# Kernel optimization log

Hardware: AMD Instinct MI355X
Metric: run time of the kernel (lower is better)

The kernel has to match this reference:

```python
import jax, jax.numpy as jnp
import numpy as np

N_NODES = 50000
N_EDGES = 800000
IN_CH = 128
HID = 128
N_LAYERS = 2


def setup_inputs() -> dict:
    key = jax.random.key(0)
    ks = jax.random.split(key, 8)
    x = jax.random.normal(ks[0], (N_NODES, IN_CH), dtype=jnp.float32)
    edge_index = jax.random.randint(ks[1], (2, N_EDGES), 0, N_NODES, dtype=jnp.int32)
    s = 1.0 / np.sqrt(IN_CH)
    lin_w = jax.random.uniform(ks[2], (IN_CH, HID), jnp.float32, -s, s)
    lin_b = jax.random.uniform(ks[3], (HID,), jnp.float32, -s, s)
    s2 = 1.0 / np.sqrt(HID)
    conv_w = jax.random.uniform(ks[4], (N_LAYERS, HID, HID), jnp.float32, -s2, s2)
    conv_b = jax.random.uniform(ks[5], (N_LAYERS, HID), jnp.float32, -s2, s2)
    return {"x": x, "edge_index": edge_index, "lin_w": lin_w, "lin_b": lin_b,
            "conv_w": conv_w, "conv_b": conv_b}


def _gcn_conv(h, src, dst, deg_inv_sqrt, W, b):
    # GCNConv: out[i] = sum_{(j->i)} d_i^{-1/2} d_j^{-1/2} (h W)[j] + b
    # (edge list already includes self-loops; deg computed once outside)
    n = h.shape[0]
    hw = h @ W  # [N, hid]
    norm = deg_inv_sqrt[src] * deg_inv_sqrt[dst]  # [E']
    msg = hw[src] * norm[:, None]  # [E', hid] gathered + scaled messages
    out = jnp.zeros_like(hw).at[dst].add(msg)  # scatter-add aggregation
    return out + b


def reference(x, edge_index, lin_w, lin_b, conv_w, conv_b):
    n = x.shape[0]
    loops = jnp.arange(n, dtype=edge_index.dtype)
    src = jnp.concatenate([edge_index[0], loops])  # add self-loops
    dst = jnp.concatenate([edge_index[1], loops])
    deg = jnp.zeros((n,), x.dtype).at[dst].add(1.0)  # in-degree incl. self-loop
    deg_inv_sqrt = jax.lax.rsqrt(deg)  # deg >= 1, no inf

    h = jax.nn.relu(x @ lin_w + lin_b)
    for l in range(conv_w.shape[0]):
        h = jax.nn.relu(_gcn_conv(h, src, dst, deg_inv_sqrt, conv_w[l], conv_b[l]))
        # dropout: identity in inference/reference mode
    return h
```

## Files before the change

### kernel.cpp

```cpp
#include <hip/hip_runtime.h>


typedef __attribute__((ext_vector_type(8))) short short8;
typedef __attribute__((ext_vector_type(4))) float floatx4;

static __device__ __forceinline__ unsigned short f2bf(float x) {
    unsigned int u = __builtin_bit_cast(unsigned int, x);
    unsigned int r = (u + 0x7fffu + ((u >> 16) & 1u)) >> 16;
    return (unsigned short)r;
}
static __device__ __forceinline__ float bflo(unsigned int u) {
    return __builtin_bit_cast(float, u << 16);
}
static __device__ __forceinline__ float bfhi(unsigned int u) {
    return __builtin_bit_cast(float, u & 0xffff0000u);
}

__global__ __launch_bounds__(256) void deg_kernel(const int* __restrict__ dst,
                                                  int* __restrict__ deg,
                                                  int* __restrict__ rank, int E) {
    int e = blockIdx.x * 256 + threadIdx.x;
    if (e < E) rank[e] = atomicAdd(&deg[dst[e]], 1);
}

__global__ __launch_bounds__(256) void scan_part(const int* __restrict__ deg,
                                                 int* __restrict__ bsum,
                                                 float* __restrict__ dis, int n) {
    __shared__ int lds[256];
    const int tid = threadIdx.x;
    const int base = blockIdx.x * 1024 + tid * 4;
    int s = 0;
    if (base + 3 < n) {
        int4 v = *(const int4*)(deg + base);
        s = v.x + v.y + v.z + v.w;
        float4 d;
        d.x = rsqrtf((float)v.x + 1.0f);
        d.y = rsqrtf((float)v.y + 1.0f);
        d.z = rsqrtf((float)v.z + 1.0f);
        d.w = rsqrtf((float)v.w + 1.0f);
        *(float4*)(dis + base) = d;
    } else {
#pragma unroll
        for (int j = 0; j < 4; ++j)
            if (base + j < n) {
                int dv = deg[base + j];
                s += dv;
                dis[base + j] = rsqrtf((float)dv + 1.0f);
            }
    }
    lds[tid] = s;
    __syncthreads();
    for (int off = 128; off > 0; off >>= 1) {
        if (tid < off) lds[tid] += lds[tid + off];
        __syncthreads();
    }
    if (tid == 0) bsum[blockIdx.x] = lds[0];
}

__global__ __launch_bounds__(64) void scan_bsum(int* __restrict__ bsum, int nb) {
    const int lane = threadIdx.x;
    int carry = 0;
    for (int b0 = 0; b0 < nb; b0 += 64) {
        int i = b0 + lane;
        int orig = (i < nb) ? bsum[i] : 0;
        int v = orig;
#pragma unroll
        for (int off = 1; off < 64; off <<= 1) {
            int u = __shfl_up(v, off);
            if (lane >= off) v += u;
        }
        int total = __shfl(v, 63);
        if (i < nb) bsum[i] = carry + v - orig;
        carry += total;
    }
}

__global__ __launch_bounds__(256) void scan_final(const int* __restrict__ deg,
                                                  const int* __restrict__ bsum,
                                                  int* __restrict__ row_off,
                                                  int n, int total) {
    __shared__ int lds[256];
    const int tid = threadIdx.x;
    const int base = blockIdx.x * 1024 + tid * 4;
    int d[4];
    int s = 0;
#pragma unroll
    for (int j = 0; j < 4; ++j) {
        d[j] = (base + j < n) ? deg[base + j] : 0;
        s += d[j];
    }
    lds[tid] = s;
    __syncthreads();
    for (int off = 1; off < 256; off <<= 1) {
        int v = (tid >= off) ? lds[tid - off] : 0;
        __syncthreads();
        lds[tid] += v;
        __syncthreads();
    }
    int run = bsum[blockIdx.x] + (lds[tid] - s);
#pragma unroll
    for (int j = 0; j < 4; ++j) {
        if (base + j < n) { row_off[base + j] = run; run += d[j]; }
    }
    if (blockIdx.x == 0 && tid == 0) row_off[n] = total;
}

__global__ __launch_bounds__(256) void csr_fill(const int* __restrict__ src,
                                                const int* __restrict__ dst,
                                                const int* __restrict__ rank,
                                                const int* __restrict__ row_off,
                                                int* __restrict__ csr, int E) {
    int e = blockIdx.x * 256 + threadIdx.x;
    if (e < E) csr[row_off[dst[e]] + rank[e]] = src[e];
}

__global__ __launch_bounds__(256) void prep_w(const float* __restrict__ lin_w,
                                              const float* __restrict__ conv_w,
                                              unsigned short* __restrict__ wt) {
    int t = blockIdx.x * 256 + threadIdx.x;
    int mat = t >> 14;
    int idx = t & 16383;
    int c = idx >> 7, k = idx & 127;
    const float* srcw = (mat == 0) ? lin_w : conv_w + (size_t)(mat - 1) * 16384;
    wt[(size_t)mat * 16384 + c * 128 + k] = f2bf(srcw[k * 128 + c]);
}

template <int MODE>
__global__ __launch_bounds__(256) void mm_mfma(const float* __restrict__ A,
                                               const unsigned short* __restrict__ Wt,
                                               const float* __restrict__ bias,
                                               const float* __restrict__ dis,
                                               float* __restrict__ Cf,
                                               unsigned short* __restrict__ Cb,
                                               int M) {
    __shared__ alignas(16) short As[128 * 128];
    __shared__ alignas(16) short Ws[128 * 128];

    const int tid = threadIdx.x;
    const int m0 = blockIdx.x * 128;

#pragma unroll
    for (int i = 0; i < 8; ++i) {
        int t = i * 256 + tid;
        int row = t >> 4;
        int k = (t & 15) * 8;
        int sidx = row * 128 + (k ^ ((row & 7) << 3));
        int gr = m0 + row;
        if (gr >= M) gr = M - 1;
        const float4* ap = (const float4*)(A + (size_t)gr * 128 + k);
        float4 x0 = ap[0], x1 = ap[1];
        short8 ua;
        ua[0] = (short)f2bf(x0.x); ua[1] = (short)f2bf(x0.y);
        ua[2] = (short)f2bf(x0.z); ua[3] = (short)f2bf(x0.w);
        ua[4] = (short)f2bf(x1.x); ua[5] = (short)f2bf(x1.y);
        ua[6] = (short)f2bf(x1.z); ua[7] = (short)f2bf(x1.w);
        *(short8*)&As[sidx] = ua;
        short8 uw = *(const short8*)(Wt + (size_t)row * 128 + k);
        *(short8*)&Ws[sidx] = uw;
    }
    __syncthreads();

    const int w = tid >> 6;
    const int l = tid & 63;
    const int lr = l & 15;
    const int lk = l >> 4;

    floatx4 acc[2][8];
#pragma unroll
    for (int rt = 0; rt < 2; ++rt)
#pragma unroll
        for (int ct = 0; ct < 8; ++ct) acc[rt][ct] = (floatx4){0.f, 0.f, 0.f, 0.f};

#pragma unroll
    for (int kb = 0; kb < 4; ++kb) {
        const int k = kb * 32 + lk * 8;
        short8 af[2];
#pragma unroll
        for (int rt = 0; rt < 2; ++rt) {
            int row = (w * 2 + rt) * 16 + lr;
            af[rt] = *(const short8*)&As[row * 128 + (k ^ ((row & 7) << 3))];
        }
#pragma unroll
        for (int ct = 0; ct < 8; ++ct) {
            int col = ct * 16 + lr;
            short8 bf = *(const short8*)&Ws[col * 128 + (k ^ ((col & 7) << 3))];
            acc[0][ct] = __builtin_amdgcn_mfma_f32_16x16x32_bf16(af[0], bf, acc[0][ct], 0, 0, 0);
            acc[1][ct] = __builtin_amdgcn_mfma_f32_16x16x32_bf16(af[1], bf, acc[1][ct], 0, 0, 0);
        }
    }

    float bb[8];
    if (MODE == 0) {
#pragma unroll
        for (int ct = 0; ct < 8; ++ct) bb[ct] = bias[ct * 16 + lr];
    }
#pragma unroll
    for (int rt = 0; rt < 2; ++rt) {
#pragma unroll
        for (int r = 0; r < 4; ++r) {
            int grow = m0 + (w * 2 + rt) * 16 + lk * 4 + r;
            if (grow < M) {
                if (MODE == 0) {
#pragma unroll
                    for (int ct = 0; ct < 8; ++ct) {
                        float v = fmaxf(acc[rt][ct][r] + bb[ct], 0.f);
                        Cf[(size_t)grow * 128 + ct * 16 + lr] = v;
                    }
                } else {
                    const float sc = dis[grow];
#pragma unroll
                    for (int ct = 0; ct < 8; ++ct) {
                        Cb[(size_t)grow * 128 + ct * 16 + lr] = f2bf(acc[rt][ct][r] * sc);
                    }
                }
            }
        }
    }
}

static __device__ __forceinline__ void acc8(float* acc, uint4 v) {
    acc[0] += bflo(v.x); acc[1] += bfhi(v.x);
    acc[2] += bflo(v.y); acc[3] += bfhi(v.y);
    acc[4] += bflo(v.z); acc[5] += bfhi(v.z);
    acc[6] += bflo(v.w); acc[7] += bfhi(v.w);
}

__global__ __launch_bounds__(256) void agg_bf16(const unsigned short* __restrict__ msg,
                                                const int* __restrict__ row_off,
                                                const int* __restrict__ csr,
                                                const float* __restrict__ dis,
                                                const float* __restrict__ bias,
                                                float* __restrict__ out, int n) {
    const int node = blockIdx.x * 4 + (threadIdx.x >> 6);
    const int lane = threadIdx.x & 63;
    if (node >= n) return;
    const int q = lane >> 4;
    const int l4 = lane & 15;
    const uint4* m4 = (const uint4*)msg;
    const int e0 = row_off[node];
    const int e1 = row_off[node + 1];

    float acc[8];
#pragma unroll
    for (int j = 0; j < 8; ++j) acc[j] = 0.f;

    int e = e0 + q;
    for (; e + 12 < e1; e += 16) {
        int s0 = csr[e];
        int s1 = csr[e + 4];
        int s2 = csr[e + 8];
        int s3 = csr[e + 12];
        uint4 v0 = m4[(size_t)s0 * 16 + l4];
        uint4 v1 = m4[(size_t)s1 * 16 + l4];
        uint4 v2 = m4[(size_t)s2 * 16 + l4];
        uint4 v3 = m4[(size_t)s3 * 16 + l4];
        acc8(acc, v0); acc8(acc, v1); acc8(acc, v2); acc8(acc, v3);
    }
    for (; e < e1; e += 4) {
        int s0 = csr[e];
        uint4 v0 = m4[(size_t)s0 * 16 + l4];
        acc8(acc, v0);
    }
    if (q == 0) {
        uint4 v0 = m4[(size_t)node * 16 + l4];
        acc8(acc, v0);
    }
#pragma unroll
    for (int j = 0; j < 8; ++j) {
        acc[j] += __shfl_xor(acc[j], 16);
        acc[j] += __shfl_xor(acc[j], 32);
    }
    if (lane < 16) {
        const float di = dis[node];
        float4 b0 = ((const float4*)bias)[l4 * 2];
        float4 b1 = ((const float4*)bias)[l4 * 2 + 1];
        float4 o0, o1;
        o0.x = fmaxf(fmaf(di, acc[0], b0.x), 0.f);
        o0.y = fmaxf(fmaf(di, acc[1], b0.y), 0.f);
        o0.z = fmaxf(fmaf(di, acc[2], b0.z), 0.f);
        o0.w = fmaxf(fmaf(di, acc[3], b0.w), 0.f);
        o1.x = fmaxf(fmaf(di, acc[4], b1.x), 0.f);
        o1.y = fmaxf(fmaf(di, acc[5], b1.y), 0.f);
        o1.z = fmaxf(fmaf(di, acc[6], b1.z), 0.f);
        o1.w = fmaxf(fmaf(di, acc[7], b1.w), 0.f);
        float4* orow = (float4*)(out + (size_t)node * 128);
        orow[l4 * 2] = o0;
        orow[l4 * 2 + 1] = o1;
    }
}

extern "C" void kernel_launch(void* const* d_in, const int* in_sizes, int n_in,
                              void* d_out, int out_size, void* d_ws, size_t ws_size,
                              hipStream_t stream) {
    const float* x      = (const float*)d_in[0];
    const int*   ei     = (const int*)d_in[1];
    const float* lin_w  = (const float*)d_in[2];
    const float* lin_b  = (const float*)d_in[3];
    const float* conv_w = (const float*)d_in[4];
    const float* conv_b = (const float*)d_in[5];
    float* outp = (float*)d_out;

    const int N = in_sizes[0] / 128;
    const int E = in_sizes[1] / 2;
    const int* srcp = ei;
    const int* dstp = ei + E;

    char* ws = (char*)d_ws;
    size_t off = 0;
    auto take = [&](size_t bytes) -> char* {
        char* p = ws + off;
        off = (off + bytes + 255) & ~(size_t)255;
        return p;
    };
    int*   deg     = (int*)take((size_t)N * 4);
    int*   rank    = (int*)take((size_t)E * 4);
    int*   row_off = (int*)take((size_t)(N + 1) * 4);
    float* dis     = (float*)take((size_t)N * 4);
    int*   csr     = (int*)take((size_t)E * 4);
    int*   bsum    = (int*)take((size_t)256 * 4);
    unsigned short* wt = (unsigned short*)take((size_t)3 * 16384 * 2);
    float* bufA    = (float*)take((size_t)N * 128 * 4);
    unsigned short* msg = (unsigned short*)take((size_t)N * 128 * 2);
    (void)ws_size; (void)n_in; (void)out_size;

    hipMemsetAsync(deg, 0, (size_t)N * 4, stream);

    prep_w<<<192, 256, 0, stream>>>(lin_w, conv_w, wt);
    deg_kernel<<<(E + 255) / 256, 256, 0, stream>>>(dstp, deg, rank, E);

    const int nb = (N + 1023) / 1024;
    scan_part<<<nb, 256, 0, stream>>>(deg, bsum, dis, N);
    scan_bsum<<<1, 64, 0, stream>>>(bsum, nb);
    scan_final<<<nb, 256, 0, stream>>>(deg, bsum, row_off, N, E);

    csr_fill<<<(E + 255) / 256, 256, 0, stream>>>(srcp, dstp, rank, row_off, csr, E);

    const int mb = (N + 127) / 128;
    const int ab = (N + 3) / 4;
    mm_mfma<0><<<mb, 256, 0, stream>>>(x, wt, lin_b, nullptr, bufA, nullptr, N);
    mm_mfma<1><<<mb, 256, 0, stream>>>(bufA, wt + 16384, nullptr, dis, nullptr, msg, N);
    agg_bf16<<<ab, 256, 0, stream>>>(msg, row_off, csr, dis, conv_b, bufA, N);
    mm_mfma<1><<<mb, 256, 0, stream>>>(bufA, wt + 32768, nullptr, dis, nullptr, msg, N);
    agg_bf16<<<ab, 256, 0, stream>>>(msg, row_off, csr, dis, conv_b + 128, outp, N);
}
```

Measured before the change: 240.5 us.

## Fuse input linear and first conv GEMM, store intermediate in bf16, merge prep kernels

Chains the input linear layer and the first conv matmul inside one kernel through LDS, so the fp32 hidden activation no longer makes a round trip through global memory. The first aggregation now writes bf16, and a dedicated bf16-input GEMM consumes it, halving that buffer's traffic. Weight prep is folded into the degree kernel and the block-sum scan into scan_final, which removes two launches. The cost is more LDS reuse and synchronization in the fused GEMM, plus extra bf16 rounding of the intermediate activation.

```diff
diff --git a/kernel.cpp b/kernel.cpp
--- a/kernel.cpp
+++ b/kernel.cpp
@@ -16,11 +16,22 @@
     return __builtin_bit_cast(float, u & 0xffff0000u);
 }
 
-__global__ __launch_bounds__(256) void deg_kernel(const int* __restrict__ dst,
+__global__ __launch_bounds__(256) void pre_kernel(const int* __restrict__ dst,
                                                   int* __restrict__ deg,
-                                                  int* __restrict__ rank, int E) {
+                                                  int* __restrict__ rank,
+                                                  const float* __restrict__ lin_w,
+                                                  const float* __restrict__ conv_w,
+                                                  unsigned short* __restrict__ wt,
+                                                  int E) {
     int e = blockIdx.x * 256 + threadIdx.x;
     if (e < E) rank[e] = atomicAdd(&deg[dst[e]], 1);
+    if (e < 3 * 16384) {
+        int mat = e >> 14;
+        int idx = e & 16383;
+        int c = idx >> 7, k = idx & 127;
+        const float* srcw = (mat == 0) ? lin_w : conv_w + (size_t)(mat - 1) * 16384;
+        wt[(size_t)mat * 16384 + c * 128 + k] = f2bf(srcw[k * 128 + c]);
+    }
 }
 
 __global__ __launch_bounds__(256) void scan_part(const int* __restrict__ deg,
@@ -57,30 +68,23 @@
     if (tid == 0) bsum[blockIdx.x] = lds[0];
 }
 
-__global__ __launch_bounds__(64) void scan_bsum(int* __restrict__ bsum, int nb) {
-    const int lane = threadIdx.x;
-    int carry = 0;
-    for (int b0 = 0; b0 < nb; b0 += 64) {
-        int i = b0 + lane;
-        int orig = (i < nb) ? bsum[i] : 0;
-        int v = orig;
-#pragma unroll
-        for (int off = 1; off < 64; off <<= 1) {
-            int u = __shfl_up(v, off);
-            if (lane >= off) v += u;
-        }
-        int total = __shfl(v, 63);
-        if (i < nb) bsum[i] = carry + v - orig;
-        carry += total;
-    }
-}
-
 __global__ __launch_bounds__(256) void scan_final(const int* __restrict__ deg,
                                                   const int* __restrict__ bsum,
                                                   int* __restrict__ row_off,
-                                                  int n, int total) {
+                                                  int n, int total, int nb) {
     __shared__ int lds[256];
+    __shared__ int sb[64];
     const int tid = threadIdx.x;
+    if (tid < 64) {
+        int orig = (tid < nb) ? bsum[tid] : 0;
+        int v = orig;
+#pragma unroll
+        for (int off = 1; off < 64; off <<= 1) {
+            int u = __shfl_up(v, off);
+            if (tid >= off) v += u;
+        }
+        sb[tid] = v - orig;
+    }
     const int base = blockIdx.x * 1024 + tid * 4;
     int d[4];
     int s = 0;
@@ -97,7 +101,7 @@
         lds[tid] += v;
         __syncthreads();
     }
-    int run = bsum[blockIdx.x] + (lds[tid] - s);
+    int run = sb[blockIdx.x] + (lds[tid] - s);
 #pragma unroll
     for (int j = 0; j < 4; ++j) {
         if (base + j < n) { row_off[base + j] = run; run += d[j]; }
@@ -114,30 +118,21 @@
     if (e < E) csr[row_off[dst[e]] + rank[e]] = src[e];
 }
 
-__global__ __launch_bounds__(256) void prep_w(const float* __restrict__ lin_w,
-                                              const float* __restrict__ conv_w,
-                                              unsigned short* __restrict__ wt) {
-    int t = blockIdx.x * 256 + threadIdx.x;
-    int mat = t >> 14;
-    int idx = t & 16383;
-    int c = idx >> 7, k = idx & 127;
-    const float* srcw = (mat == 0) ? lin_w : conv_w + (size_t)(mat - 1) * 16384;
-    wt[(size_t)mat * 16384 + c * 128 + k] = f2bf(srcw[k * 128 + c]);
-}
-
-template <int MODE>
-__global__ __launch_bounds__(256) void mm_mfma(const float* __restrict__ A,
-                                               const unsigned short* __restrict__ Wt,
-                                               const float* __restrict__ bias,
-                                               const float* __restrict__ dis,
-                                               float* __restrict__ Cf,
-                                               unsigned short* __restrict__ Cb,
-                                               int M) {
+__global__ __launch_bounds__(256) void mm_fused(const float* __restrict__ x,
+                                                const unsigned short* __restrict__ wt,
+                                                const float* __restrict__ lin_b,
+                                                const float* __restrict__ dis,
+                                                unsigned short* __restrict__ msg,
+                                                int M) {
     __shared__ alignas(16) short As[128 * 128];
     __shared__ alignas(16) short Ws[128 * 128];
 
     const int tid = threadIdx.x;
     const int m0 = blockIdx.x * 128;
+    const int w = tid >> 6;
+    const int l = tid & 63;
+    const int lr = l & 15;
+    const int lk = l >> 4;
 
 #pragma unroll
     for (int i = 0; i < 8; ++i) {
@@ -147,7 +142,7 @@
         int sidx = row * 128 + (k ^ ((row & 7) << 3));
         int gr = m0 + row;
         if (gr >= M) gr = M - 1;
-        const float4* ap = (const float4*)(A + (size_t)gr * 128 + k);
+        const float4* ap = (const float4*)(x + (size_t)gr * 128 + k);
         float4 x0 = ap[0], x1 = ap[1];
         short8 ua;
         ua[0] = (short)f2bf(x0.x); ua[1] = (short)f2bf(x0.y);
@@ -155,22 +150,15 @@
         ua[4] = (short)f2bf(x1.x); ua[5] = (short)f2bf(x1.y);
         ua[6] = (short)f2bf(x1.z); ua[7] = (short)f2bf(x1.w);
         *(short8*)&As[sidx] = ua;
-        short8 uw = *(const short8*)(Wt + (size_t)row * 128 + k);
-        *(short8*)&Ws[sidx] = uw;
-    }
-    __syncthreads();
-
-    const int w = tid >> 6;
-    const int l = tid & 63;
-    const int lr = l & 15;
-    const int lk = l >> 4;
+        *(short8*)&Ws[sidx] = *(const short8*)(wt + (size_t)row * 128 + k);
+    }
+    __syncthreads();
 
     floatx4 acc[2][8];
 #pragma unroll
     for (int rt = 0; rt < 2; ++rt)
 #pragma unroll
         for (int ct = 0; ct < 8; ++ct) acc[rt][ct] = (floatx4){0.f, 0.f, 0.f, 0.f};
-
 #pragma unroll
     for (int kb = 0; kb < 4; ++kb) {
         const int k = kb * 32 + lk * 8;
@@ -188,30 +176,133 @@
             acc[1][ct] = __builtin_amdgcn_mfma_f32_16x16x32_bf16(af[1], bf, acc[1][ct], 0, 0, 0);
         }
     }
+    __syncthreads();
 
     float bb[8];
-    if (MODE == 0) {
-#pragma unroll
-        for (int ct = 0; ct < 8; ++ct) bb[ct] = bias[ct * 16 + lr];
-    }
+#pragma unroll
+    for (int ct = 0; ct < 8; ++ct) bb[ct] = lin_b[ct * 16 + lr];
+#pragma unroll
+    for (int rt = 0; rt < 2; ++rt) {
+#pragma unroll
+        for (int r = 0; r < 4; ++r) {
+            int rowl = (w * 2 + rt) * 16 + lk * 4 + r;
+#pragma unroll
+            for (int ct = 0; ct < 8; ++ct) {
+                int col = ct * 16 + lr;
+                float v = fmaxf(acc[rt][ct][r] + bb[ct], 0.f);
+                As[rowl * 128 + (col ^ ((rowl & 7) << 3))] = (short)f2bf(v);
+            }
+        }
+    }
+#pragma unroll
+    for (int i = 0; i < 8; ++i) {
+        int t = i * 256 + tid;
+        int row = t >> 4;
+        int k = (t & 15) * 8;
+        int sidx = row * 128 + (k ^ ((row & 7) << 3));
+        *(short8*)&Ws[sidx] = *(const short8*)(wt + 16384 + (size_t)row * 128 + k);
+    }
+    __syncthreads();
+
+#pragma unroll
+    for (int rt = 0; rt < 2; ++rt)
+#pragma unroll
+        for (int ct = 0; ct < 8; ++ct) acc[rt][ct] = (floatx4){0.f, 0.f, 0.f, 0.f};
+#pragma unroll
+    for (int kb = 0; kb < 4; ++kb) {
+        const int k = kb * 32 + lk * 8;
+        short8 af[2];
+#pragma unroll
+        for (int rt = 0; rt < 2; ++rt) {
+            int row = (w * 2 + rt) * 16 + lr;
+            af[rt] = *(const short8*)&As[row * 128 + (k ^ ((row & 7) << 3))];
+        }
+#pragma unroll
+        for (int ct = 0; ct < 8; ++ct) {
+            int col = ct * 16 + lr;
+            short8 bf = *(const short8*)&Ws[col * 128 + (k ^ ((col & 7) << 3))];
+            acc[0][ct] = __builtin_amdgcn_mfma_f32_16x16x32_bf16(af[0], bf, acc[0][ct], 0, 0, 0);
+            acc[1][ct] = __builtin_amdgcn_mfma_f32_16x16x32_bf16(af[1], bf, acc[1][ct], 0, 0, 0);
+        }
+    }
+
 #pragma unroll
     for (int rt = 0; rt < 2; ++rt) {
 #pragma unroll
         for (int r = 0; r < 4; ++r) {
             int grow = m0 + (w * 2 + rt) * 16 + lk * 4 + r;
             if (grow < M) {
-                if (MODE == 0) {
-#pragma unroll
-                    for (int ct = 0; ct < 8; ++ct) {
-                        float v = fmaxf(acc[rt][ct][r] + bb[ct], 0.f);
-                        Cf[(size_t)grow * 128 + ct * 16 + lr] = v;
-                    }
-                } else {
-                    const float sc = dis[grow];
-#pragma unroll
-                    for (int ct = 0; ct < 8; ++ct) {
-                        Cb[(size_t)grow * 128 + ct * 16 + lr] = f2bf(acc[rt][ct][r] * sc);
-                    }
+                const float sc = dis[grow];
+#pragma unroll
+                for (int ct = 0; ct < 8; ++ct) {
+                    msg[(size_t)grow * 128 + ct * 16 + lr] = f2bf(acc[rt][ct][r] * sc);
+                }
+            }
+        }
+    }
+}
+
+__global__ __launch_bounds__(256) void mm_h1(const unsigned short* __restrict__ h1,
+                                             const unsigned short* __restrict__ wt2,
+                                             const float* __restrict__ dis,
+                                             unsigned short* __restrict__ msg,
+                                             int M) {
+    __shared__ alignas(16) short As[128 * 128];
+    __shared__ alignas(16) short Ws[128 * 128];
+
+    const int tid = threadIdx.x;
+    const int m0 = blockIdx.x * 128;
+
+#pragma unroll
+    for (int i = 0; i < 8; ++i) {
+        int t = i * 256 + tid;
+        int row = t >> 4;
+        int k = (t & 15) * 8;
+        int sidx = row * 128 + (k ^ ((row & 7) << 3));
+        int gr = m0 + row;
+        if (gr >= M) gr = M - 1;
+        *(short8*)&As[sidx] = *(const short8*)(h1 + (size_t)gr * 128 + k);
+        *(short8*)&Ws[sidx] = *(const short8*)(wt2 + (size_t)row * 128 + k);
+    }
+    __syncthreads();
+
+    const int w = tid >> 6;
+    const int l = tid & 63;
+    const int lr = l & 15;
+    const int lk = l >> 4;
+
+    floatx4 acc[2][8];
+#pragma unroll
+    for (int rt = 0; rt < 2; ++rt)
+#pragma unroll
+        for (int ct = 0; ct < 8; ++ct) acc[rt][ct] = (floatx4){0.f, 0.f, 0.f, 0.f};
+#pragma unroll
+    for (int kb = 0; kb < 4; ++kb) {
+        const int k = kb * 32 + lk * 8;
+        short8 af[2];
+#pragma unroll
+        for (int rt = 0; rt < 2; ++rt) {
+            int row = (w * 2 + rt) * 16 + lr;
+            af[rt] = *(const short8*)&As[row * 128 + (k ^ ((row & 7) << 3))];
+        }
+#pragma unroll
+        for (int ct = 0; ct < 8; ++ct) {
+            int col = ct * 16 + lr;
+            short8 bf = *(const short8*)&Ws[col * 128 + (k ^ ((col & 7) << 3))];
+            acc[0][ct] = __builtin_amdgcn_mfma_f32_16x16x32_bf16(af[0], bf, acc[0][ct], 0, 0, 0);
+            acc[1][ct] = __builtin_amdgcn_mfma_f32_16x16x32_bf16(af[1], bf, acc[1][ct], 0, 0, 0);
+        }
+    }
+#pragma unroll
+    for (int rt = 0; rt < 2; ++rt) {
+#pragma unroll
+        for (int r = 0; r < 4; ++r) {
+            int grow = m0 + (w * 2 + rt) * 16 + lk * 4 + r;
+            if (grow < M) {
+                const float sc = dis[grow];
+#pragma unroll
+                for (int ct = 0; ct < 8; ++ct) {
+                    msg[(size_t)grow * 128 + ct * 16 + lr] = f2bf(acc[rt][ct][r] * sc);
                 }
             }
         }
@@ -225,12 +316,13 @@
     acc[6] += bflo(v.w); acc[7] += bfhi(v.w);
 }
 
+template <int OUT_BF16>
 __global__ __launch_bounds__(256) void agg_bf16(const unsigned short* __restrict__ msg,
                                                 const int* __restrict__ row_off,
                                                 const int* __restrict__ csr,
                                                 const float* __restrict__ dis,
                                                 const float* __restrict__ bias,
-                                                float* __restrict__ out, int n) {
+                                                void* __restrict__ outv, int n) {
     const int node = blockIdx.x * 4 + (threadIdx.x >> 6);
     const int lane = threadIdx.x & 63;
     if (node >= n) return;
@@ -274,18 +366,25 @@
         const float di = dis[node];
         float4 b0 = ((const float4*)bias)[l4 * 2];
         float4 b1 = ((const float4*)bias)[l4 * 2 + 1];
-        float4 o0, o1;
-        o0.x = fmaxf(fmaf(di, acc[0], b0.x), 0.f);
-        o0.y = fmaxf(fmaf(di, acc[1], b0.y), 0.f);
-        o0.z = fmaxf(fmaf(di, acc[2], b0.z), 0.f);
-        o0.w = fmaxf(fmaf(di, acc[3], b0.w), 0.f);
-        o1.x = fmaxf(fmaf(di, acc[4], b1.x), 0.f);
-        o1.y = fmaxf(fmaf(di, acc[5], b1.y), 0.f);
-        o1.z = fmaxf(fmaf(di, acc[6], b1.z), 0.f);
-        o1.w = fmaxf(fmaf(di, acc[7], b1.w), 0.f);
-        float4* orow = (float4*)(out + (size_t)node * 128);
-        orow[l4 * 2] = o0;
-        orow[l4 * 2 + 1] = o1;
+        float o[8];
+        o[0] = fmaxf(fmaf(di, acc[0], b0.x), 0.f);
+        o[1] = fmaxf(fmaf(di, acc[1], b0.y), 0.f);
+        o[2] = fmaxf(fmaf(di, acc[2], b0.z), 0.f);
+        o[3] = fmaxf(fmaf(di, acc[3], b0.w), 0.f);
+        o[4] = fmaxf(fmaf(di, acc[4], b1.x), 0.f);
+        o[5] = fmaxf(fmaf(di, acc[5], b1.y), 0.f);
+        o[6] = fmaxf(fmaf(di, acc[6], b1.z), 0.f);
+        o[7] = fmaxf(fmaf(di, acc[7], b1.w), 0.f);
+        if (OUT_BF16) {
+            short8 p;
+#pragma unroll
+            for (int j = 0; j < 8; ++j) p[j] = (short)f2bf(o[j]);
+            *(short8*)((unsigned short*)outv + (size_t)node * 128 + l4 * 8) = p;
+        } else {
+            float4* orow = (float4*)((float*)outv + (size_t)node * 128);
+            orow[l4 * 2] = make_float4(o[0], o[1], o[2], o[3]);
+            orow[l4 * 2 + 1] = make_float4(o[4], o[5], o[6], o[7]);
+        }
     }
 }
 
@@ -318,28 +417,25 @@
     float* dis     = (float*)take((size_t)N * 4);
     int*   csr     = (int*)take((size_t)E * 4);
     int*   bsum    = (int*)take((size_t)256 * 4);
-    unsigned short* wt = (unsigned short*)take((size_t)3 * 16384 * 2);
-    float* bufA    = (float*)take((size_t)N * 128 * 4);
+    unsigned short* wt  = (unsigned short*)take((size_t)3 * 16384 * 2);
+    unsigned short* h1  = (unsigned short*)take((size_t)N * 128 * 2);
     unsigned short* msg = (unsigned short*)take((size_t)N * 128 * 2);
     (void)ws_size; (void)n_in; (void)out_size;
 
     hipMemsetAsync(deg, 0, (size_t)N * 4, stream);
 
-    prep_w<<<192, 256, 0, stream>>>(lin_w, conv_w, wt);
-    deg_kernel<<<(E + 255) / 256, 256, 0, stream>>>(dstp, deg, rank, E);
+    pre_kernel<<<(E + 255) / 256, 256, 0, stream>>>(dstp, deg, rank, lin_w, conv_w, wt, E);
 
     const int nb = (N + 1023) / 1024;
     scan_part<<<nb, 256, 0, stream>>>(deg, bsum, dis, N);
-    scan_bsum<<<1, 64, 0, stream>>>(bsum, nb);
-    scan_final<<<nb, 256, 0, stream>>>(deg, bsum, row_off, N, E);
+    scan_final<<<nb, 256, 0, stream>>>(deg, bsum, row_off, N, E, nb);
 
     csr_fill<<<(E + 255) / 256, 256, 0, stream>>>(srcp, dstp, rank, row_off, csr, E);
 
     const int mb = (N + 127) / 128;
     const int ab = (N + 3) / 4;
-    mm_mfma<0><<<mb, 256, 0, stream>>>(x, wt, lin_b, nullptr, bufA, nullptr, N);
-    mm_mfma<1><<<mb, 256, 0, stream>>>(bufA, wt + 16384, nullptr, dis, nullptr, msg, N);
-    agg_bf16<<<ab, 256, 0, stream>>>(msg, row_off, csr, dis, conv_b, bufA, N);
-    mm_mfma<1><<<mb, 256, 0, stream>>>(bufA, wt + 32768, nullptr, dis, nullptr, msg, N);
-    agg_bf16<<<ab, 256, 0, stream>>>(msg, row_off, csr, dis, conv_b + 128, outp, N);
-}
+    mm_fused<<<mb, 256, 0, stream>>>(x, wt, lin_b, dis, msg, N);
+    agg_bf16<1><<<ab, 256, 0, stream>>>(msg, row_off, csr, dis, conv_b, h1, N);
+    mm_h1<<<mb, 256, 0, stream>>>(h1, wt + 32768, dis, msg, N);
+    agg_bf16<0><<<ab, 256, 0, stream>>>(msg, row_off, csr, dis, conv_b + 128, outp, N);
+}
```

New measurement: 231.7 us. -3.7%, faster.
